# Kernel optimization log

Hardware: AMD Instinct MI355X
Metric: run time of the kernel (lower is better)

Reference implementation:

```python
import jax, jax.numpy as jnp
import numpy as np

N = 100000      # nodes
R = 4           # relations
E = 500000      # edges per relation
IN, HID, OUT = 256, 128, 64


def _graphconv(x, src, dst, W, b, n_nodes):
    """DGL GraphConv, norm='both': D_dst^{-1/2} A (D_src^{-1/2} x) W + b.
    Transform-first (in_feats >= out_feats path); math identical either way."""
    e = src.shape[0]
    ones = jnp.ones((e,), x.dtype)
    deg_out = jnp.clip(jax.ops.segment_sum(ones, src, num_segments=n_nodes), 1.0)
    deg_in = jnp.clip(jax.ops.segment_sum(ones, dst, num_segments=n_nodes), 1.0)
    h = (x * jax.lax.rsqrt(deg_out)[:, None]) @ W           # [N, out]
    agg = jax.ops.segment_sum(h[src], dst, num_segments=n_nodes)  # scatter-add over edges
    return agg * jax.lax.rsqrt(deg_in)[:, None] + b


def _hetero_layer(x, edges_src, edges_dst, W, b, n_nodes):
    # HeteroGraphConv(aggregate='sum'): sum of per-relation GraphConv outputs
    out = _graphconv(x, edges_src[0], edges_dst[0], W[0], b[0], n_nodes)
    for r in range(1, W.shape[0]):
        out = out + _graphconv(x, edges_src[r], edges_dst[r], W[r], b[r], n_nodes)
    return out


def setup_inputs() -> dict:
    key = jax.random.key(0)
    ks = jax.random.split(key, 8)
    x = jax.random.normal(ks[0], (N, IN), dtype=jnp.float32)
    edges_src = jax.random.randint(ks[1], (R, E), 0, N, dtype=jnp.int32)
    edges_dst = jax.random.randint(ks[2], (R, E), 0, N, dtype=jnp.int32)
    s1 = 1.0 / np.sqrt(IN)
    s2 = 1.0 / np.sqrt(HID)
    W1 = jax.random.uniform(ks[3], (R, IN, HID), jnp.float32, -s1, s1)
    b1 = jnp.zeros((R, HID), jnp.float32)
    W2 = jax.random.uniform(ks[4], (R, HID, OUT), jnp.float32, -s2, s2)
    b2 = jnp.zeros((R, OUT), jnp.float32)
    return {"x": x, "edges_src": edges_src, "edges_dst": edges_dst,
            "W1": W1, "b1": b1, "W2": W2, "b2": b2}


def reference(x, edges_src, edges_dst, W1, b1, W2, b2):
    h = _hetero_layer(x, edges_src, edges_dst, W1, b1, N)
    h = jax.nn.relu(h)
    out = _hetero_layer(h, edges_src, edges_dst, W2, b2, N)
    return out
```

## Files before the change

### kernel.cpp

```cpp
#include <hip/hip_runtime.h>

#define NN   100000
#define RR   4
#define EE   500000
#define FIN  256
#define FHID 128
#define FOUT 64
#define NBLK ((NN + 255) / 256)
#define NPAD (NN + 32)

#define PEDGE  ((RR * EE + 255) / 256)
#define PER9   (9 * PEDGE)
#define PCW1   (RR * FIN * FHID / 256)
#define PCW2   (RR * FHID * FOUT / 256)
#define PREP_GRID (PER9 + PCW1 + PCW2 + 1)

#define NG1    ((NN + 127) / 128 * 4)
#define GF_PER 1564
#define GF_GRID (7 * GF_PER)

typedef unsigned short u16;
typedef unsigned char  u8;
typedef unsigned int   u32;
typedef __attribute__((ext_vector_type(8))) __bf16 bf16x8;
typedef __attribute__((ext_vector_type(4))) float  f32x4;
typedef __attribute__((ext_vector_type(4))) u32    u32x4;

__device__ __forceinline__ u16 f2bf(float f) {
    union { float f; u32 u; } v; v.f = f;
    u32 r = v.u + 0x7FFFu + ((v.u >> 16) & 1u);
    return (u16)(r >> 16);
}

__device__ __forceinline__ float2 bfx2(u32 v) {
    union { u32 u; float f; } a, b;
    a.u = v << 16; b.u = v & 0xFFFF0000u;
    return {a.f, b.f};
}

typedef __attribute__((address_space(3))) u32 lds_u32;
typedef __attribute__((address_space(1))) const u32 gl_u32;
__device__ __forceinline__ void gload16(const void* g, void* l) {
    __builtin_amdgcn_global_load_lds((gl_u32*)g, (lds_u32*)l, 16, 0, 0);
}

__global__ __launch_bounds__(256) void prep_mega(
        const float2* __restrict__ x2, u32* __restrict__ Xbf2,
        const float* __restrict__ W1, u16* __restrict__ W1t,
        const float* __restrict__ W2, u16* __restrict__ W2t,
        const int* __restrict__ esrc, const int* __restrict__ edst,
        u32* __restrict__ counto, u32* __restrict__ counti,
        u8* __restrict__ pos8,
        const float* __restrict__ b1, const float* __restrict__ b2,
        float* __restrict__ sb1, float* __restrict__ sb2) {
    int bx = blockIdx.x, t = threadIdx.x;
    if (bx < PER9) {
        int p = bx / 9, q = bx - p * 9;
        if (q == 0) {
            int i = p * 256 + t;
            if (i < RR * EE) {
                int r = i / EE;
                atomicAdd(&counto[esrc[i]], 1u << (8 * r));
            }
        } else if (q == 1) {
            int i = p * 256 + t;
            if (i < RR * EE) {
                int r = i / EE;
                u32 old = atomicAdd(&counti[edst[i]], 1u << (8 * r));
                pos8[i] = (u8)((old >> (8 * r)) & 255u);
            }
        } else {
            int i = (p * 7 + (q - 2)) * 256 + t;
            if (i < NN * FIN / 2) {
                float2 f = x2[i];
                Xbf2[i] = ((u32)f2bf(f.y) << 16) | (u32)f2bf(f.x);
            }
        }
    } else if (bx < PER9 + PCW1) {
        int i = (bx - PER9) * 256 + t;
        int r = i / (FIN * FHID);
        int rem = i - r * FIN * FHID;
        int k = rem / FHID, n = rem - k * FHID;
        W1t[((size_t)r * FHID + n) * FIN + k] = f2bf(W1[i]);
    } else if (bx < PER9 + PCW1 + PCW2) {
        int i = (bx - PER9 - PCW1) * 256 + t;
        int r = i / (FHID * FOUT);
        int rem = i - r * FHID * FOUT;
        int k = rem / FOUT, n = rem - k * FOUT;
        W2t[((size_t)r * FOUT + n) * FHID + k] = f2bf(W2[i]);
    } else {
        if (t < FHID) {
            float v = 0.f;
            for (int r = 0; r < RR; ++r) v += b1[r * FHID + t];
            sb1[t] = v;
        } else if (t < FHID + FOUT) {
            int j = t - FHID;
            float v = 0.f;
            for (int r = 0; r < RR; ++r) v += b2[r * FOUT + j];
            sb2[j] = v;
        }
    }
}

__global__ __launch_bounds__(256) void reduce_deg(const u32* __restrict__ counto,
                                                  const u32* __restrict__ counti,
                                                  f32x4* __restrict__ so,
                                                  f32x4* __restrict__ si,
                                                  u32x4* __restrict__ di4,
                                                  int* __restrict__ cnt,
                                                  int* __restrict__ bsum) {
    __shared__ int sh[256];
    int n = blockIdx.x * 256 + threadIdx.x;
    int c = 0;
    if (n < NN) {
        u32 o = counto[n], d = counti[n];
        u32x4 dd;
        f32x4 vo, vi;
#pragma unroll
        for (int k = 0; k < 4; ++k) {
            u32 ob = (o >> (8 * k)) & 255u;
            u32 db = (d >> (8 * k)) & 255u;
            dd[k] = db;
            vo[k] = rsqrtf((float)max(ob, 1u));
            vi[k] = rsqrtf((float)max(db, 1u));
            c += (int)db;
        }
        so[n] = vo; si[n] = vi; di4[n] = dd;
        cnt[n] = c;
    }
    sh[threadIdx.x] = c;
    __syncthreads();
    for (int d = 128; d > 0; d >>= 1) {
        if (threadIdx.x < d) sh[threadIdx.x] += sh[threadIdx.x + d];
        __syncthreads();
    }
    if (threadIdx.x == 0) bsum[blockIdx.x] = sh[0];
}

__global__ __launch_bounds__(512) void scanb_kernel(const int* __restrict__ bsum,
                                                    int* __restrict__ boff) {
    __shared__ int sh[512];
    int t = threadIdx.x;
    int v = (t < NBLK) ? bsum[t] : 0;
    sh[t] = v;
    __syncthreads();
    for (int d = 1; d < 512; d <<= 1) {
        int u = (t >= d) ? sh[t - d] : 0;
        __syncthreads();
        sh[t] += u;
        __syncthreads();
    }
    if (t < NBLK) boff[t] = sh[t] - v;
}

__global__ __launch_bounds__(256) void offsets_kernel(const int* __restrict__ cnt,
                                                      const int* __restrict__ boff,
                                                      const u32x4* __restrict__ di4,
                                                      int* __restrict__ off,
                                                      u32x4* __restrict__ off4) {
    __shared__ int sh[256];
    int i = blockIdx.x * 256 + threadIdx.x;
    int t = threadIdx.x;
    int v = (i < NN) ? cnt[i] : 0;
    sh[t] = v;
    __syncthreads();
    for (int d = 1; d < 256; d <<= 1) {
        int u = (t >= d) ? sh[t - d] : 0;
        __syncthreads();
        sh[t] += u;
        __syncthreads();
    }
    int ex = boff[blockIdx.x] + sh[t] - v;
    if (i < NN) {
        off[i] = ex;
        u32x4 d = di4[i];
        u32x4 c;
        c[0] = (u32)ex;
        c[1] = c[0] + d[0];
        c[2] = c[1] + d[1];
        c[3] = c[2] + d[2];
        off4[i] = c;
    }
    if (i == NN - 1) off[NN] = ex + v;
}

template<int NW, int K, int LOG2F>
__device__ __forceinline__ void gemm_body(u16* As, u16* Bs,
                                          const u16* __restrict__ A,
                                          const u16* __restrict__ Bt,
                                          const f32x4* __restrict__ so,
                                          u16* __restrict__ Y, int M,
                                          int m0, int n0) {
    int tid = threadIdx.x;
    int wave = tid >> 6, lane = tid & 63;
    int quad = lane >> 4, l15 = lane & 15;
    int wm = (wave >> 1) * 64, wn = (wave & 1) * 64;

    int srow = tid >> 2;
    int scol = (tid & 3) * 8;
    const u16* Ag0 = A + (size_t)min(m0 + srow,      M - 1) * K + scol;
    const u16* Ag1 = A + (size_t)min(m0 + srow + 64, M - 1) * K + scol;
    const u16* Bg0 = Bt + (size_t)(n0 + srow) * K + scol;
    const u16* Bg1 = Bt + (size_t)(n0 + srow + 64) * K + scol;
    u16* As0 = As + tid * 8;
    u16* As1 = As + 2048 + tid * 8;
    u16* Bs0 = Bs + tid * 8;
    u16* Bs1 = Bs + 2048 + tid * 8;

    const bf16x8* Ard = (const bf16x8*)(As + (wm + l15) * 32 + quad * 8);
    const bf16x8* Brd = (const bf16x8*)(Bs + (wn + l15) * 32 + quad * 8);

    f32x4 acc[4][4] = {};
    for (int k0 = 0; k0 < K; k0 += 32) {
        gload16(Ag0 + k0, As0);
        gload16(Ag1 + k0, As1);
        gload16(Bg0 + k0, Bs0);
        gload16(Bg1 + k0, Bs1);
        __syncthreads();
        bf16x8 af[4], bfr[4];
#pragma unroll
        for (int i = 0; i < 4; ++i) af[i]  = Ard[i * 64];
#pragma unroll
        for (int j = 0; j < 4; ++j) bfr[j] = Brd[j * 64];
#pragma unroll
        for (int i = 0; i < 4; ++i)
#pragma unroll
            for (int j = 0; j < 4; ++j)
                acc[i][j] = __builtin_amdgcn_mfma_f32_16x16x32_bf16(af[i], bfr[j], acc[i][j], 0, 0, 0);
        __syncthreads();
    }

#pragma unroll
    for (int i = 0; i < 4; ++i) {
#pragma unroll
        for (int r = 0; r < 4; ++r) {
            int row = m0 + wm + i * 16 + quad * 4 + r;
            if (row < M) {
                f32x4 so4 = so[row];
#pragma unroll
                for (int j = 0; j < 4; ++j) {
                    int colb = n0 + wn + j * 16;
                    float scale = so4[colb >> LOG2F];
                    Y[(size_t)row * NW + colb + l15] = f2bf(acc[i][j][r] * scale);
                }
            }
        }
    }
}

template<int NW, int K, int LOG2F>
__global__ __launch_bounds__(256) void gemm_tile(const u16* __restrict__ A,
                                                 const u16* __restrict__ Bt,
                                                 const f32x4* __restrict__ so,
                                                 u16* __restrict__ Y, int M) {
    __shared__ u16 As[128 * 32];
    __shared__ u16 Bs[128 * 32];
    gemm_body<NW, K, LOG2F>(As, Bs, A, Bt, so, Y, M, blockIdx.x * 128, blockIdx.y * 128);
}

__global__ __launch_bounds__(256) void gemm_place(const u16* __restrict__ A,
                                                  const u16* __restrict__ Bt,
                                                  const f32x4* __restrict__ so,
                                                  u16* __restrict__ Y, int M,
                                                  const int* __restrict__ esrc,
                                                  const int* __restrict__ edst,
                                                  const u32* __restrict__ off4,
                                                  const u8* __restrict__ pos8,
                                                  u32* __restrict__ meta) {
    __shared__ u16 As[128 * 32];
    __shared__ u16 Bs[128 * 32];
    int p = blockIdx.x / 7, q = blockIdx.x - p * 7;
    if (q < 2) {
        int gb = p * 2 + q;
        if (gb >= NG1) return;
        gemm_body<RR * FHID, FIN, 7>(As, Bs, A, Bt, so, Y, M,
                                     (gb >> 2) * 128, (gb & 3) * 128);
    } else {
        int i = (p * 5 + (q - 2)) * 256 + threadIdx.x;
        if (i >= RR * EE) return;
        int r = i / EE;
        int s = esrc[i], d = edst[i];
        u32 pos = pos8[i];
        meta[off4[d * 4 + r] + pos] = (u32)(s * 4 + r);
    }
}


__global__ __launch_bounds__(256) void gather1(const u32* __restrict__ Y,
                                               const int* __restrict__ off,
                                               const u32* __restrict__ meta,
                                               const f32x4* __restrict__ si,
                                               const float* __restrict__ sb,
                                               u32* __restrict__ H1) {
    int wid  = blockIdx.x * 4 + (threadIdx.x >> 6);
    int lane = threadIdx.x & 63;
    if (wid >= NN) return;
    int j = off[wid], end = off[wid + 1];
    f32x4 si4 = si[wid];
    float a0x = 0.f, a0y = 0.f, a1x = 0.f, a1y = 0.f;
    float a2x = 0.f, a2y = 0.f, a3x = 0.f, a3y = 0.f;
    for (; j + 4 <= end; j += 4) {
        u32 m0 = meta[j], m1 = meta[j + 1], m2 = meta[j + 2], m3 = meta[j + 3];
        u32 v0 = Y[(size_t)m0 * 64 + lane];
        u32 v1 = Y[(size_t)m1 * 64 + lane];
        u32 v2 = Y[(size_t)m2 * 64 + lane];
        u32 v3 = Y[(size_t)m3 * 64 + lane];
        float2 f0 = bfx2(v0), f1 = bfx2(v1), f2 = bfx2(v2), f3 = bfx2(v3);
        float c0 = si4[m0 & 3], c1 = si4[m1 & 3], c2 = si4[m2 & 3], c3 = si4[m3 & 3];
        a0x = fmaf(c0, f0.x, a0x); a0y = fmaf(c0, f0.y, a0y);
        a1x = fmaf(c1, f1.x, a1x); a1y = fmaf(c1, f1.y, a1y);
        a2x = fmaf(c2, f2.x, a2x); a2y = fmaf(c2, f2.y, a2y);
        a3x = fmaf(c3, f3.x, a3x); a3y = fmaf(c3, f3.y, a3y);
    }
    for (; j < end; ++j) {
        u32 m0 = meta[j];
        u32 v0 = Y[(size_t)m0 * 64 + lane];
        float2 f0 = bfx2(v0);
        float c0 = si4[m0 & 3];
        a0x = fmaf(c0, f0.x, a0x); a0y = fmaf(c0, f0.y, a0y);
    }
    float2 b = ((const float2*)sb)[lane];
    float ax = fmaxf((a0x + a1x) + (a2x + a3x) + b.x, 0.f);
    float ay = fmaxf((a0y + a1y) + (a2y + a3y) + b.y, 0.f);
    H1[(size_t)wid * 64 + lane] = ((u32)f2bf(ay) << 16) | (u32)f2bf(ax);
}

__global__ __launch_bounds__(256) void gather2(const u32* __restrict__ Y,
                                               const int* __restrict__ off,
                                               const u32* __restrict__ meta,
                                               const f32x4* __restrict__ si,
                                               const float* __restrict__ sb,
                                               float* __restrict__ out) {
    int wid  = blockIdx.x * 4 + (threadIdx.x >> 6);
    int lane = threadIdx.x & 63;
    if (wid >= NN) return;
    int sub = lane >> 5, col = lane & 31;
    int end = off[wid + 1];
    int j = off[wid] + sub;
    f32x4 si4 = si[wid];
    float a0x = 0.f, a0y = 0.f, a1x = 0.f, a1y = 0.f;
    for (; j + 2 < end; j += 4) {
        u32 m0 = meta[j], m1 = meta[j + 2];
        u32 v0 = Y[(size_t)m0 * 32 + col];
        u32 v1 = Y[(size_t)m1 * 32 + col];
        float2 f0 = bfx2(v0), f1 = bfx2(v1);
        float c0 = si4[m0 & 3], c1 = si4[m1 & 3];
        a0x = fmaf(c0, f0.x, a0x); a0y = fmaf(c0, f0.y, a0y);
        a1x = fmaf(c1, f1.x, a1x); a1y = fmaf(c1, f1.y, a1y);
    }
    if (j < end) {
        u32 m0 = meta[j];
        u32 v0 = Y[(size_t)m0 * 32 + col];
        float2 f0 = bfx2(v0);
        float c0 = si4[m0 & 3];
        a0x = fmaf(c0, f0.x, a0x); a0y = fmaf(c0, f0.y, a0y);
    }
    float ax = a0x + a1x, ay = a0y + a1y;
    ax += __shfl_xor(ax, 32);
    ay += __shfl_xor(ay, 32);
    if (sub == 0) {
        float2 b = ((const float2*)sb)[col];
        float2 o = {ax + b.x, ay + b.y};
        ((float2*)out)[(size_t)wid * 32 + col] = o;
    }
}


extern "C" void kernel_launch(void* const* d_in, const int* in_sizes, int n_in,
                              void* d_out, int out_size, void* d_ws, size_t ws_size,
                              hipStream_t stream) {
    const float* x    = (const float*)d_in[0];
    const int*   esrc = (const int*)  d_in[1];
    const int*   edst = (const int*)  d_in[2];
    const float* W1   = (const float*)d_in[3];
    const float* b1   = (const float*)d_in[4];
    const float* W2   = (const float*)d_in[5];
    const float* b2   = (const float*)d_in[6];
    float* out = (float*)d_out;

    char* w = (char*)d_ws;
    auto alloc = [&](size_t bytes) -> char* {
        char* p = w; w += (bytes + 255) & ~(size_t)255; return p;
    };
    u32*   cnt2    = (u32*)  alloc((size_t)2 * NPAD * 4);
    u32*   counto  = cnt2;
    u32*   counti  = cnt2 + NPAD;
    float* so      = (float*)alloc((size_t)NN * 4 * 4);
    float* si      = (float*)alloc((size_t)NN * 4 * 4);
    u32*   di4     = (u32*)  alloc((size_t)NN * 4 * 4);
    int*   cnt     = (int*)  alloc((size_t)NN * 4);
    int*   off     = (int*)  alloc((size_t)(NN + 1) * 4);
    u32*   off4    = (u32*)  alloc((size_t)NN * 4 * 4);
    int*   bsum    = (int*)  alloc((size_t)NBLK * 4);
    int*   boff    = (int*)  alloc((size_t)NBLK * 4);
    float* sb1     = (float*)alloc(FHID * 4);
    float* sb2     = (float*)alloc(FOUT * 4);
    u8*    pos8    = (u8*)   alloc((size_t)RR * EE);
    u16*   W1t     = (u16*)  alloc((size_t)RR * FIN * FHID * 2);
    u16*   W2t     = (u16*)  alloc((size_t)RR * FHID * FOUT * 2);
    u32*   meta    = (u32*)  alloc((size_t)RR * EE * 4);
    u16*   Xbf     = (u16*)  alloc((size_t)NN * FIN * 2);
    u16*   Yall    = (u16*)  alloc((size_t)NN * RR * FHID * 2);
    u16*   H1bf    = Xbf;

    hipMemsetAsync(cnt2, 0, (size_t)2 * NPAD * 4, stream);

    prep_mega<<<PREP_GRID, 256, 0, stream>>>((const float2*)x, (u32*)Xbf,
                                             W1, W1t, W2, W2t, esrc, edst,
                                             counto, counti, pos8, b1, b2, sb1, sb2);
    reduce_deg<<<NBLK, 256, 0, stream>>>(counto, counti,
                                         (f32x4*)so, (f32x4*)si, (u32x4*)di4, cnt, bsum);
    scanb_kernel<<<1, 512, 0, stream>>>(bsum, boff);
    offsets_kernel<<<NBLK, 256, 0, stream>>>(cnt, boff, (const u32x4*)di4, off, (u32x4*)off4);

    gemm_place<<<GF_GRID, 256, 0, stream>>>(Xbf, W1t, (const f32x4*)so, Yall, NN,
                                            esrc, edst, off4, pos8, meta);
    gather1<<<(NN + 3) / 4, 256, 0, stream>>>((const u32*)Yall, off, meta,
                                              (const f32x4*)si, sb1, (u32*)H1bf);

    {
        dim3 grid((NN + 127) / 128, (RR * FOUT) / 128);
        gemm_tile<RR * FOUT, FHID, 6><<<grid, 256, 0, stream>>>(H1bf, W2t, (const f32x4*)so, Yall, NN);
    }
    gather2<<<(NN + 3) / 4, 256, 0, stream>>>((const u32*)Yall, off, meta,
                                              (const f32x4*)si, sb2, out);
}
```

Measured before the change: 567.5 us.

## Fuse x bf16 conversion into layer-1 GEMM and overlap it with degree counting

The layer-1 GEMM now reads the fp32 input directly and converts it to bf16 while staging tiles into LDS, so the separate Xbf conversion pass and its extra read and write of x go away. The D_src^{-1/2} scaling moves from the GEMM epilogue into gather1, which lets the GEMM run before degrees are known. The GEMM is co-scheduled with the edge degree-count atomics in one kernel, and edge placement becomes its own kernel. In exchange, each A tile load now does fp32 loads plus register conversion, and gather1 does an extra per-edge so lookup and multiply.

```diff
diff --git a/kernel.cpp b/kernel.cpp
--- a/kernel.cpp
+++ b/kernel.cpp
@@ -10,14 +10,13 @@
 #define NPAD (NN + 32)
 
 #define PEDGE  ((RR * EE + 255) / 256)
-#define PER9   (9 * PEDGE)
 #define PCW1   (RR * FIN * FHID / 256)
 #define PCW2   (RR * FHID * FOUT / 256)
-#define PREP_GRID (PER9 + PCW1 + PCW2 + 1)
+#define CONVW_GRID (PCW1 + PCW2 + 1)
 
 #define NG1    ((NN + 127) / 128 * 4)
-#define GF_PER 1564
-#define GF_GRID (7 * GF_PER)
+#define K1_PER 1564
+#define K1_GRID (7 * K1_PER)
 
 typedef unsigned short u16;
 typedef unsigned char  u8;
@@ -31,6 +30,9 @@
     u32 r = v.u + 0x7FFFu + ((v.u >> 16) & 1u);
     return (u16)(r >> 16);
 }
+__device__ __forceinline__ u32 pack2bf(float x, float y) {
+    return ((u32)f2bf(y) << 16) | (u32)f2bf(x);
+}
 
 __device__ __forceinline__ float2 bfx2(u32 v) {
     union { u32 u; float f; } a, b;
@@ -44,46 +46,20 @@
     __builtin_amdgcn_global_load_lds((gl_u32*)g, (lds_u32*)l, 16, 0, 0);
 }
 
-__global__ __launch_bounds__(256) void prep_mega(
-        const float2* __restrict__ x2, u32* __restrict__ Xbf2,
+__global__ __launch_bounds__(256) void convw_kernel(
         const float* __restrict__ W1, u16* __restrict__ W1t,
         const float* __restrict__ W2, u16* __restrict__ W2t,
-        const int* __restrict__ esrc, const int* __restrict__ edst,
-        u32* __restrict__ counto, u32* __restrict__ counti,
-        u8* __restrict__ pos8,
         const float* __restrict__ b1, const float* __restrict__ b2,
         float* __restrict__ sb1, float* __restrict__ sb2) {
     int bx = blockIdx.x, t = threadIdx.x;
-    if (bx < PER9) {
-        int p = bx / 9, q = bx - p * 9;
-        if (q == 0) {
-            int i = p * 256 + t;
-            if (i < RR * EE) {
-                int r = i / EE;
-                atomicAdd(&counto[esrc[i]], 1u << (8 * r));
-            }
-        } else if (q == 1) {
-            int i = p * 256 + t;
-            if (i < RR * EE) {
-                int r = i / EE;
-                u32 old = atomicAdd(&counti[edst[i]], 1u << (8 * r));
-                pos8[i] = (u8)((old >> (8 * r)) & 255u);
-            }
-        } else {
-            int i = (p * 7 + (q - 2)) * 256 + t;
-            if (i < NN * FIN / 2) {
-                float2 f = x2[i];
-                Xbf2[i] = ((u32)f2bf(f.y) << 16) | (u32)f2bf(f.x);
-            }
-        }
-    } else if (bx < PER9 + PCW1) {
-        int i = (bx - PER9) * 256 + t;
+    if (bx < PCW1) {
+        int i = bx * 256 + t;
         int r = i / (FIN * FHID);
         int rem = i - r * FIN * FHID;
         int k = rem / FHID, n = rem - k * FHID;
         W1t[((size_t)r * FHID + n) * FIN + k] = f2bf(W1[i]);
-    } else if (bx < PER9 + PCW1 + PCW2) {
-        int i = (bx - PER9 - PCW1) * 256 + t;
+    } else if (bx < PCW1 + PCW2) {
+        int i = (bx - PCW1) * 256 + t;
         int r = i / (FHID * FOUT);
         int rem = i - r * FHID * FOUT;
         int k = rem / FOUT, n = rem - k * FOUT;
@@ -102,6 +78,97 @@
     }
 }
 
+__device__ __forceinline__ void gemm1_body(u16* As, u16* Bs,
+                                           const float* __restrict__ X,
+                                           const u16* __restrict__ Bt,
+                                           u16* __restrict__ Y, int M,
+                                           int m0, int n0) {
+    int tid = threadIdx.x;
+    int wave = tid >> 6, lane = tid & 63;
+    int quad = lane >> 4, l15 = lane & 15;
+    int wm = (wave >> 1) * 64, wn = (wave & 1) * 64;
+
+    int arow = tid >> 1;
+    int acol = (tid & 1) * 16;
+    const float4* Ag = (const float4*)(X + (size_t)min(m0 + arow, M - 1) * FIN + acol);
+    u32* Aw = (u32*)As + arow * 16 + (acol >> 1);
+
+    int srow = tid >> 2;
+    int scol = (tid & 3) * 8;
+    const u16* Bg0 = Bt + (size_t)(n0 + srow) * FIN + scol;
+    const u16* Bg1 = Bt + (size_t)(n0 + srow + 64) * FIN + scol;
+    u16* Bs0 = Bs + tid * 8;
+    u16* Bs1 = Bs + 2048 + tid * 8;
+
+    const bf16x8* Ard = (const bf16x8*)(As + (wm + l15) * 32 + quad * 8);
+    const bf16x8* Brd = (const bf16x8*)(Bs + (wn + l15) * 32 + quad * 8);
+
+    f32x4 acc[4][4] = {};
+    for (int k0 = 0; k0 < FIN; k0 += 32) {
+        gload16(Bg0 + k0, Bs0);
+        gload16(Bg1 + k0, Bs1);
+        float4 f0 = Ag[(k0 >> 2) + 0], f1 = Ag[(k0 >> 2) + 1];
+        float4 f2 = Ag[(k0 >> 2) + 2], f3 = Ag[(k0 >> 2) + 3];
+        u32x4 w0 = {pack2bf(f0.x, f0.y), pack2bf(f0.z, f0.w),
+                    pack2bf(f1.x, f1.y), pack2bf(f1.z, f1.w)};
+        u32x4 w1 = {pack2bf(f2.x, f2.y), pack2bf(f2.z, f2.w),
+                    pack2bf(f3.x, f3.y), pack2bf(f3.z, f3.w)};
+        ((u32x4*)Aw)[0] = w0;
+        ((u32x4*)Aw)[1] = w1;
+        __syncthreads();
+        bf16x8 af[4], bfr[4];
+#pragma unroll
+        for (int i = 0; i < 4; ++i) af[i]  = Ard[i * 64];
+#pragma unroll
+        for (int j = 0; j < 4; ++j) bfr[j] = Brd[j * 64];
+#pragma unroll
+        for (int i = 0; i < 4; ++i)
+#pragma unroll
+            for (int j = 0; j < 4; ++j)
+                acc[i][j] = __builtin_amdgcn_mfma_f32_16x16x32_bf16(af[i], bfr[j], acc[i][j], 0, 0, 0);
+        __syncthreads();
+    }
+
+#pragma unroll
+    for (int i = 0; i < 4; ++i) {
+#pragma unroll
+        for (int r = 0; r < 4; ++r) {
+            int row = m0 + wm + i * 16 + quad * 4 + r;
+            if (row < M) {
+#pragma unroll
+                for (int j = 0; j < 4; ++j) {
+                    int col = n0 + wn + j * 16 + l15;
+                    Y[(size_t)row * (RR * FHID) + col] = f2bf(acc[i][j][r]);
+                }
+            }
+        }
+    }
+}
+
+__global__ __launch_bounds__(256) void count_gemm(
+        const float* __restrict__ x, const u16* __restrict__ W1t,
+        u16* __restrict__ Y,
+        const int* __restrict__ esrc, const int* __restrict__ edst,
+        u32* __restrict__ counto, u32* __restrict__ counti,
+        u8* __restrict__ pos8) {
+    __shared__ u16 As[128 * 32];
+    __shared__ u16 Bs[128 * 32];
+    int p = blockIdx.x / 7, q = blockIdx.x - p * 7;
+    if (q < 2) {
+        int gb = p * 2 + q;
+        if (gb >= NG1) return;
+        gemm1_body(As, Bs, x, W1t, Y, NN, (gb >> 2) * 128, (gb & 3) * 128);
+    } else {
+        int i = (p * 5 + (q - 2)) * 256 + threadIdx.x;
+        if (i >= RR * EE) return;
+        int r = i / EE;
+        int s = esrc[i], d = edst[i];
+        atomicAdd(&counto[s], 1u << (8 * r));
+        u32 old = atomicAdd(&counti[d], 1u << (8 * r));
+        pos8[i] = (u8)((old >> (8 * r)) & 255u);
+    }
+}
+
 __global__ __launch_bounds__(256) void reduce_deg(const u32* __restrict__ counto,
                                                   const u32* __restrict__ counti,
                                                   f32x4* __restrict__ so,
@@ -184,14 +251,26 @@
     if (i == NN - 1) off[NN] = ex + v;
 }
 
+__global__ __launch_bounds__(256) void place_kernel(const int* __restrict__ esrc,
+                                                    const int* __restrict__ edst,
+                                                    const u32* __restrict__ off4,
+                                                    const u8* __restrict__ pos8,
+                                                    u32* __restrict__ meta) {
+    int i = blockIdx.x * 256 + threadIdx.x;
+    if (i >= RR * EE) return;
+    int r = i / EE;
+    meta[off4[edst[i] * 4 + r] + pos8[i]] = (u32)(esrc[i] * 4 + r);
+}
+
 template<int NW, int K, int LOG2F>
-__device__ __forceinline__ void gemm_body(u16* As, u16* Bs,
-                                          const u16* __restrict__ A,
-                                          const u16* __restrict__ Bt,
-                                          const f32x4* __restrict__ so,
-                                          u16* __restrict__ Y, int M,
-                                          int m0, int n0) {
+__global__ __launch_bounds__(256) void gemm_tile(const u16* __restrict__ A,
+                                                 const u16* __restrict__ Bt,
+                                                 const f32x4* __restrict__ so,
+                                                 u16* __restrict__ Y, int M) {
+    __shared__ u16 As[128 * 32];
+    __shared__ u16 Bs[128 * 32];
     int tid = threadIdx.x;
+    int m0 = blockIdx.x * 128, n0 = blockIdx.y * 128;
     int wave = tid >> 6, lane = tid & 63;
     int quad = lane >> 4, l15 = lane & 15;
     int wm = (wave >> 1) * 64, wn = (wave & 1) * 64;
@@ -248,47 +327,11 @@
     }
 }
 
-template<int NW, int K, int LOG2F>
-__global__ __launch_bounds__(256) void gemm_tile(const u16* __restrict__ A,
-                                                 const u16* __restrict__ Bt,
-                                                 const f32x4* __restrict__ so,
-                                                 u16* __restrict__ Y, int M) {
-    __shared__ u16 As[128 * 32];
-    __shared__ u16 Bs[128 * 32];
-    gemm_body<NW, K, LOG2F>(As, Bs, A, Bt, so, Y, M, blockIdx.x * 128, blockIdx.y * 128);
-}
-
-__global__ __launch_bounds__(256) void gemm_place(const u16* __restrict__ A,
-                                                  const u16* __restrict__ Bt,
-                                                  const f32x4* __restrict__ so,
-                                                  u16* __restrict__ Y, int M,
-                                                  const int* __restrict__ esrc,
-                                                  const int* __restrict__ edst,
-                                                  const u32* __restrict__ off4,
-                                                  const u8* __restrict__ pos8,
-                                                  u32* __restrict__ meta) {
-    __shared__ u16 As[128 * 32];
-    __shared__ u16 Bs[128 * 32];
-    int p = blockIdx.x / 7, q = blockIdx.x - p * 7;
-    if (q < 2) {
-        int gb = p * 2 + q;
-        if (gb >= NG1) return;
-        gemm_body<RR * FHID, FIN, 7>(As, Bs, A, Bt, so, Y, M,
-                                     (gb >> 2) * 128, (gb & 3) * 128);
-    } else {
-        int i = (p * 5 + (q - 2)) * 256 + threadIdx.x;
-        if (i >= RR * EE) return;
-        int r = i / EE;
-        int s = esrc[i], d = edst[i];
-        u32 pos = pos8[i];
-        meta[off4[d * 4 + r] + pos] = (u32)(s * 4 + r);
-    }
-}
-
 
 __global__ __launch_bounds__(256) void gather1(const u32* __restrict__ Y,
                                                const int* __restrict__ off,
                                                const u32* __restrict__ meta,
+                                               const float* __restrict__ soF,
                                                const f32x4* __restrict__ si,
                                                const float* __restrict__ sb,
                                                u32* __restrict__ H1) {
@@ -305,8 +348,9 @@
         u32 v1 = Y[(size_t)m1 * 64 + lane];
         u32 v2 = Y[(size_t)m2 * 64 + lane];
         u32 v3 = Y[(size_t)m3 * 64 + lane];
+        float c0 = soF[m0] * si4[m0 & 3], c1 = soF[m1] * si4[m1 & 3];
+        float c2 = soF[m2] * si4[m2 & 3], c3 = soF[m3] * si4[m3 & 3];
         float2 f0 = bfx2(v0), f1 = bfx2(v1), f2 = bfx2(v2), f3 = bfx2(v3);
-        float c0 = si4[m0 & 3], c1 = si4[m1 & 3], c2 = si4[m2 & 3], c3 = si4[m3 & 3];
         a0x = fmaf(c0, f0.x, a0x); a0y = fmaf(c0, f0.y, a0y);
         a1x = fmaf(c1, f1.x, a1x); a1y = fmaf(c1, f1.y, a1y);
         a2x = fmaf(c2, f2.x, a2x); a2y = fmaf(c2, f2.y, a2y);
@@ -316,7 +360,7 @@
         u32 m0 = meta[j];
         u32 v0 = Y[(size_t)m0 * 64 + lane];
         float2 f0 = bfx2(v0);
-        float c0 = si4[m0 & 3];
+        float c0 = soF[m0] * si4[m0 & 3];
         a0x = fmaf(c0, f0.x, a0x); a0y = fmaf(c0, f0.y, a0y);
     }
     float2 b = ((const float2*)sb)[lane];
@@ -399,24 +443,24 @@
     u16*   W1t     = (u16*)  alloc((size_t)RR * FIN * FHID * 2);
     u16*   W2t     = (u16*)  alloc((size_t)RR * FHID * FOUT * 2);
     u32*   meta    = (u32*)  alloc((size_t)RR * EE * 4);
-    u16*   Xbf     = (u16*)  alloc((size_t)NN * FIN * 2);
+    u16*   H1bf    = (u16*)  alloc((size_t)NN * FHID * 2);
     u16*   Yall    = (u16*)  alloc((size_t)NN * RR * FHID * 2);
-    u16*   H1bf    = Xbf;
 
     hipMemsetAsync(cnt2, 0, (size_t)2 * NPAD * 4, stream);
 
-    prep_mega<<<PREP_GRID, 256, 0, stream>>>((const float2*)x, (u32*)Xbf,
-                                             W1, W1t, W2, W2t, esrc, edst,
-                                             counto, counti, pos8, b1, b2, sb1, sb2);
+    convw_kernel<<<CONVW_GRID, 256, 0, stream>>>(W1, W1t, W2, W2t, b1, b2, sb1, sb2);
+
+    count_gemm<<<K1_GRID, 256, 0, stream>>>(x, W1t, Yall, esrc, edst,
+                                            counto, counti, pos8);
+
     reduce_deg<<<NBLK, 256, 0, stream>>>(counto, counti,
                                          (f32x4*)so, (f32x4*)si, (u32x4*)di4, cnt, bsum);
     scanb_kernel<<<1, 512, 0, stream>>>(bsum, boff);
     offsets_kernel<<<NBLK, 256, 0, stream>>>(cnt, boff, (const u32x4*)di4, off, (u32x4*)off4);
-
-    gemm_place<<<GF_GRID, 256, 0, stream>>>(Xbf, W1t, (const f32x4*)so, Yall, NN,
-                                            esrc, edst, off4, pos8, meta);
+    place_kernel<<<PEDGE, 256, 0, stream>>>(esrc, edst, off4, pos8, meta);
+
     gather1<<<(NN + 3) / 4, 256, 0, stream>>>((const u32*)Yall, off, meta,
-                                              (const f32x4*)si, sb1, (u32*)H1bf);
+                                              so, (const f32x4*)si, sb1, (u32*)H1bf);
 
     {
         dim3 grid((NN + 127) / 128, (RR * FOUT) / 128);
```

Measured after the change: 551.4 us. -2.9%, faster.
